# Kernel optimization log

Measured on AMD Instinct MI355X. Metric: run time of the kernel, lower is better.

## Reference

```python
import math
import jax, jax.numpy as jnp
import numpy as np

B, Q, K, D, H, C = 4, 1024, 1024, 256, 8, 32  # batch, q_len, kv_len, model dim, heads, per-head dim


def setup_inputs() -> dict:
    key = jax.random.key(0)
    ks = jax.random.split(key, 9)
    s = 1.0 / math.sqrt(D)
    return {
        "q_x": jax.random.normal(ks[0], (B, Q, D), jnp.float32),
        "kv_x": jax.random.normal(ks[1], (B, K, D), jnp.float32),
        "bias_mask": jax.random.normal(ks[2], (B, 1, 1, K), jnp.float32),
        "bias_pair": jax.random.normal(ks[3], (B, H, Q, K), jnp.float32),
        "wq": jax.random.normal(ks[4], (D, H * C), jnp.float32) * s,
        "wk": jax.random.normal(ks[5], (D, H * C), jnp.float32) * s,
        "wv": jax.random.normal(ks[6], (D, H * C), jnp.float32) * s,
        "wg": jnp.zeros((D, H * C), jnp.float32),  # gating init: weights 0
        "bg": jnp.ones((H * C,), jnp.float32),     # gating init: bias 1
        "wo": jax.random.normal(ks[7], (H * C, D), jnp.float32) * s,
        "bo": jnp.zeros((D,), jnp.float32),
    }


def reference(q_x, kv_x, bias_mask, bias_pair, wq, wk, wv, wg, bg, wo, bo):
    # project and split heads: [B, L, H, C]
    q = (q_x @ wq).reshape(B, Q, H, C) / math.sqrt(C)
    k = (kv_x @ wk).reshape(B, K, H, C)
    v = (kv_x @ wv).reshape(B, K, H, C)
    # scores [B, H, Q, K] with multiple additive biases
    scores = jnp.einsum("bqhc,bkhc->bhqk", q, k) + bias_mask + bias_pair
    a = jax.nn.softmax(scores, axis=-1)
    o = jnp.einsum("bhqk,bkhc->bqhc", a, v).reshape(B, Q, H * C)
    # sigmoid gate from query activations
    g = jax.nn.sigmoid(q_x @ wg + bg)
    o = o * g
    return o @ wo + bo
```

## Files before the change

### kernel.cpp

```cpp
#include <hip/hip_runtime.h>
#include <hip/hip_bf16.h>


typedef short bf16x8 __attribute__((ext_vector_type(8)));
typedef float f32x4 __attribute__((ext_vector_type(4)));

__device__ __forceinline__ unsigned short f2bf(float f) {
  __hip_bfloat16 hb = __float2bfloat16(f);
  return *reinterpret_cast<const unsigned short*>(&hb);
}

__global__ __launch_bounds__(256) void transpose_conv(
    const float* __restrict__ wq, const float* __restrict__ wk,
    const float* __restrict__ wv, const float* __restrict__ wg,
    const float* __restrict__ wo, unsigned short* __restrict__ wt) {
  __shared__ float t[64][65];
  const int widx = blockIdx.x >> 4;
  const int tile = blockIdx.x & 15;
  const float* src = widx == 0 ? wq : widx == 1 ? wk
                     : widx == 2 ? wv : widx == 3 ? wg : wo;
  unsigned short* dst = wt + widx * 65536;
  const int r0 = (tile >> 2) * 64, c0 = (tile & 3) * 64;
  const int tr = threadIdx.x >> 4;
  const int tc4 = (threadIdx.x & 15) * 4;
#pragma unroll
  for (int i = 0; i < 4; ++i) {
    const float4 u = *reinterpret_cast<const float4*>(
        src + (size_t)(r0 + tr + i * 16) * 256 + c0 + tc4);
    t[tr + i * 16][tc4 + 0] = u.x;
    t[tr + i * 16][tc4 + 1] = u.y;
    t[tr + i * 16][tc4 + 2] = u.z;
    t[tr + i * 16][tc4 + 3] = u.w;
  }
  __syncthreads();
#pragma unroll
  for (int i = 0; i < 4; ++i) {
    const int rr = tr + i * 16;
    ushort4 o;
    o.x = f2bf(t[tc4 + 0][rr]);
    o.y = f2bf(t[tc4 + 1][rr]);
    o.z = f2bf(t[tc4 + 2][rr]);
    o.w = f2bf(t[tc4 + 3][rr]);
    *reinterpret_cast<ushort4*>(dst + (size_t)(c0 + rr) * 256 + r0 + tc4) = o;
  }
}

__global__ __launch_bounds__(256) void proj_mfma(
    const float* __restrict__ q_x, const float* __restrict__ kv_x,
    const unsigned short* __restrict__ wt, const float* __restrict__ bg,
    unsigned short* __restrict__ qhb, unsigned short* __restrict__ khb,
    unsigned short* __restrict__ vhb, float* __restrict__ gws) {
  const int side = blockIdx.y;
  const int m0 = blockIdx.x * 16;
  const int lane = threadIdx.x & 63;
  const int n0 = (threadIdx.x >> 6) * 64;
  const int mrow = lane & 15;
  const int quad = lane >> 4;
  const float* X = side ? kv_x : q_x;
  const unsigned short* W0 = wt + (side ? 1 : 0) * 65536;
  const unsigned short* W1 = wt + (side ? 2 : 3) * 65536;
  f32x4 acc0[4], acc1[4];
  const f32x4 z = {0.f, 0.f, 0.f, 0.f};
#pragma unroll
  for (int nt = 0; nt < 4; ++nt) { acc0[nt] = z; acc1[nt] = z; }

  for (int k0 = 0; k0 < 256; k0 += 32) {
    const size_t abase = (size_t)(m0 + mrow) * 256 + k0 + quad * 8;
    const float4 a0 = *reinterpret_cast<const float4*>(X + abase);
    const float4 a1 = *reinterpret_cast<const float4*>(X + abase + 4);
    bf16x8 a;
    a[0] = (short)f2bf(a0.x); a[1] = (short)f2bf(a0.y);
    a[2] = (short)f2bf(a0.z); a[3] = (short)f2bf(a0.w);
    a[4] = (short)f2bf(a1.x); a[5] = (short)f2bf(a1.y);
    a[6] = (short)f2bf(a1.z); a[7] = (short)f2bf(a1.w);
#pragma unroll
    for (int nt = 0; nt < 4; ++nt) {
      const size_t wrow = (size_t)(n0 + nt * 16 + mrow) * 256 + k0 + quad * 8;
      const bf16x8 b0 = *reinterpret_cast<const bf16x8*>(W0 + wrow);
      const bf16x8 b1 = *reinterpret_cast<const bf16x8*>(W1 + wrow);
      acc0[nt] = __builtin_amdgcn_mfma_f32_16x16x32_bf16(a, b0, acc0[nt], 0, 0, 0);
      acc1[nt] = __builtin_amdgcn_mfma_f32_16x16x32_bf16(a, b1, acc1[nt], 0, 0, 0);
    }
  }

  const int b = m0 >> 10;
#pragma unroll
  for (int nt = 0; nt < 4; ++nt) {
    const int n = n0 + nt * 16 + mrow;
    const int h = n >> 5, c = n & 31;
    const float bgv = (side == 0) ? bg[n] : 0.f;
#pragma unroll
    for (int r = 0; r < 4; ++r) {
      const int row = m0 + quad * 4 + r;
      const int qp = row & 1023;
      const size_t o = ((size_t)(b * 8 + h) * 1024 + qp) * 32 + c;
      if (side == 0) {
        qhb[o] = f2bf(acc0[nt][r] * 0.17677669529663689f);
        const float zz = acc1[nt][r] + bgv;
        gws[(size_t)row * 256 + n] = 1.0f / (1.0f + __expf(-zz));
      } else {
        khb[o] = f2bf(acc0[nt][r]);
        vhb[o] = f2bf(acc1[nt][r]);
      }
    }
  }
}

__global__ __launch_bounds__(256) void attn_mfma(
    const unsigned short* __restrict__ qhb,
    const unsigned short* __restrict__ khb,
    const unsigned short* __restrict__ vhb,
    const float* __restrict__ bias_mask,
    const float* __restrict__ bias_pair,
    const float* __restrict__ gws, unsigned short* __restrict__ og) {
  __shared__ unsigned short ks[64 * 40];
  __shared__ unsigned short vsT[32 * 72];
  __shared__ unsigned short ps[64 * 72];
  const int x = blockIdx.x;
  const int b = x >> 7, h = (x >> 4) & 7, q0 = (x & 15) * 64;
  const int tid = threadIdx.x;
  const int wv = tid >> 6, lane = tid & 63, quad = lane >> 4, lr = lane & 15;
  const int bh = b * 8 + h;

  const bf16x8 aq = *reinterpret_cast<const bf16x8*>(
      qhb + ((size_t)bh * 1024 + q0 + wv * 16 + lr) * 32 + quad * 8);

  float m[4], l[4];
  f32x4 oa[2];
  const f32x4 zero4 = {0.f, 0.f, 0.f, 0.f};
  oa[0] = zero4; oa[1] = zero4;
#pragma unroll
  for (int r = 0; r < 4; ++r) { m[r] = -3e30f; l[r] = 0.f; }

  const float* bp = bias_pair + ((size_t)bh * 1024 + q0 + wv * 16) * 1024;
  const float* bm = bias_mask + (size_t)b * 1024;

  for (int kt = 0; kt < 16; ++kt) {
    const int kk0 = kt * 64;
    __syncthreads();
    {
      const unsigned short* ksrc = khb + (size_t)bh * 32768 + kk0 * 32;
      const int row = tid >> 2, c8 = (tid & 3) * 8;
      *reinterpret_cast<bf16x8*>(ks + row * 40 + c8) =
          *reinterpret_cast<const bf16x8*>(ksrc + row * 32 + c8);
      const unsigned short* vsrc = vhb + (size_t)bh * 32768 + kk0 * 32;
      const bf16x8 vv = *reinterpret_cast<const bf16x8*>(vsrc + row * 32 + c8);
#pragma unroll
      for (int i = 0; i < 8; ++i) vsT[(c8 + i) * 72 + row] = (unsigned short)vv[i];
    }
    __syncthreads();

    f32x4 s[4];
    float mk[4];
#pragma unroll
    for (int nt = 0; nt < 4; ++nt) mk[nt] = bm[kk0 + 16 * nt + lr];
#pragma unroll
    for (int nt = 0; nt < 4; ++nt) {
#pragma unroll
      for (int r = 0; r < 4; ++r)
        s[nt][r] = bp[(size_t)(quad * 4 + r) * 1024 + kk0 + 16 * nt + lr] + mk[nt];
      const bf16x8 bk = *reinterpret_cast<const bf16x8*>(
          ks + (16 * nt + lr) * 40 + quad * 8);
      s[nt] = __builtin_amdgcn_mfma_f32_16x16x32_bf16(aq, bk, s[nt], 0, 0, 0);
    }

#pragma unroll
    for (int r = 0; r < 4; ++r) {
      float mx = fmaxf(fmaxf(s[0][r], s[1][r]), fmaxf(s[2][r], s[3][r]));
      mx = fmaxf(mx, __shfl_xor(mx, 1));
      mx = fmaxf(mx, __shfl_xor(mx, 2));
      mx = fmaxf(mx, __shfl_xor(mx, 4));
      mx = fmaxf(mx, __shfl_xor(mx, 8));
      const float mn = fmaxf(m[r], mx);
      const float alpha = __expf(m[r] - mn);
      float rs = 0.f;
#pragma unroll
      for (int nt = 0; nt < 4; ++nt) {
        s[nt][r] = __expf(s[nt][r] - mn);
        rs += s[nt][r];
      }
      rs += __shfl_xor(rs, 1);
      rs += __shfl_xor(rs, 2);
      rs += __shfl_xor(rs, 4);
      rs += __shfl_xor(rs, 8);
      l[r] = l[r] * alpha + rs;
      m[r] = mn;
      oa[0][r] *= alpha;
      oa[1][r] *= alpha;
      const int ri = wv * 16 + quad * 4 + r;
#pragma unroll
      for (int nt = 0; nt < 4; ++nt)
        ps[ri * 72 + 16 * nt + lr] = f2bf(s[nt][r]);
    }
    asm volatile("s_waitcnt lgkmcnt(0)" ::: "memory");

#pragma unroll
    for (int k0i = 0; k0i < 2; ++k0i) {
      const bf16x8 ap = *reinterpret_cast<const bf16x8*>(
          ps + (wv * 16 + lr) * 72 + k0i * 32 + quad * 8);
#pragma unroll
      for (int nt2 = 0; nt2 < 2; ++nt2) {
        const bf16x8 bv = *reinterpret_cast<const bf16x8*>(
            vsT + (nt2 * 16 + lr) * 72 + k0i * 32 + quad * 8);
        oa[nt2] = __builtin_amdgcn_mfma_f32_16x16x32_bf16(ap, bv, oa[nt2], 0, 0, 0);
      }
    }
  }

#pragma unroll
  for (int r = 0; r < 4; ++r) {
    const int qr = q0 + wv * 16 + quad * 4 + r;
    const float inv = 1.0f / l[r];
    const size_t base = ((size_t)b * 1024 + qr) * 256 + h * 32;
#pragma unroll
    for (int nt2 = 0; nt2 < 2; ++nt2) {
      const int c = nt2 * 16 + lr;
      og[base + c] = f2bf(oa[nt2][r] * inv * gws[base + c]);
    }
  }
}

__global__ __launch_bounds__(256) void outproj_mfma(
    const unsigned short* __restrict__ og,
    const unsigned short* __restrict__ wt,
    const float* __restrict__ bo, float* __restrict__ out) {
  const int m0 = blockIdx.x * 16;
  const int lane = threadIdx.x & 63;
  const int n0 = (threadIdx.x >> 6) * 64;
  const int mrow = lane & 15;
  const int quad = lane >> 4;
  const unsigned short* W = wt + 4 * 65536;
  f32x4 acc[4];
  const f32x4 z = {0.f, 0.f, 0.f, 0.f};
#pragma unroll
  for (int nt = 0; nt < 4; ++nt) acc[nt] = z;

  for (int k0 = 0; k0 < 256; k0 += 32) {
    const bf16x8 a = *reinterpret_cast<const bf16x8*>(
        og + (size_t)(m0 + mrow) * 256 + k0 + quad * 8);
#pragma unroll
    for (int nt = 0; nt < 4; ++nt) {
      const bf16x8 b = *reinterpret_cast<const bf16x8*>(
          W + (size_t)(n0 + nt * 16 + mrow) * 256 + k0 + quad * 8);
      acc[nt] = __builtin_amdgcn_mfma_f32_16x16x32_bf16(a, b, acc[nt], 0, 0, 0);
    }
  }

#pragma unroll
  for (int nt = 0; nt < 4; ++nt) {
    const int n = n0 + nt * 16 + mrow;
    const float bov = bo[n];
#pragma unroll
    for (int r = 0; r < 4; ++r) {
      const int row = m0 + quad * 4 + r;
      out[(size_t)row * 256 + n] = acc[nt][r] + bov;
    }
  }
}

extern "C" void kernel_launch(void* const* d_in, const int* in_sizes, int n_in,
                              void* d_out, int out_size, void* d_ws,
                              size_t ws_size, hipStream_t stream) {
  (void)in_sizes; (void)n_in; (void)out_size; (void)ws_size;
  const float* q_x = (const float*)d_in[0];
  const float* kv_x = (const float*)d_in[1];
  const float* bias_mask = (const float*)d_in[2];
  const float* bias_pair = (const float*)d_in[3];
  const float* wq = (const float*)d_in[4];
  const float* wk = (const float*)d_in[5];
  const float* wv = (const float*)d_in[6];
  const float* wg = (const float*)d_in[7];
  const float* bg = (const float*)d_in[8];
  const float* wo = (const float*)d_in[9];
  const float* bo = (const float*)d_in[10];

  char* wsb = (char*)d_ws;
  unsigned short* wt  = (unsigned short*)(wsb);
  unsigned short* qhb = (unsigned short*)(wsb + 655360);
  unsigned short* khb = (unsigned short*)(wsb + 2752512);
  unsigned short* vhb = (unsigned short*)(wsb + 4849664);
  unsigned short* og  = (unsigned short*)(wsb + 6946816);
  float* gws          = (float*)(wsb + 9043968);

  transpose_conv<<<80, 256, 0, stream>>>(wq, wk, wv, wg, wo, wt);
  proj_mfma<<<dim3(256, 2), 256, 0, stream>>>(q_x, kv_x, wt, bg, qhb, khb,
                                              vhb, gws);
  attn_mfma<<<512, 256, 0, stream>>>(qhb, khb, vhb, bias_mask, bias_pair, gws,
                                     og);
  outproj_mfma<<<256, 256, 0, stream>>>(og, wt, bo, (float*)d_out);
}
```

Before: 252.9 us.

## Store V transposed and load K/V fragments directly from global in attention

The projection kernel now writes V in a [bh, c, k] transposed layout. The attention kernel drops the shared-memory staging of K and V, and with it both __syncthreads per tile. Each wave reads K and V MFMA operands straight from global memory (L2-cached) and keeps only a private per-wave P buffer in LDS. This removes block-level barriers and the LDS transpose. The cost is redundant global loads across the four waves and strided scattered stores of V in the projection.

```diff
diff --git a/kernel.cpp b/kernel.cpp
--- a/kernel.cpp
+++ b/kernel.cpp
@@ -49,7 +49,7 @@
     const float* __restrict__ q_x, const float* __restrict__ kv_x,
     const unsigned short* __restrict__ wt, const float* __restrict__ bg,
     unsigned short* __restrict__ qhb, unsigned short* __restrict__ khb,
-    unsigned short* __restrict__ vhb, float* __restrict__ gws) {
+    unsigned short* __restrict__ vhT, float* __restrict__ gws) {
   const int side = blockIdx.y;
   const int m0 = blockIdx.x * 16;
   const int lane = threadIdx.x & 63;
@@ -88,19 +88,20 @@
   for (int nt = 0; nt < 4; ++nt) {
     const int n = n0 + nt * 16 + mrow;
     const int h = n >> 5, c = n & 31;
+    const int bh = b * 8 + h;
     const float bgv = (side == 0) ? bg[n] : 0.f;
 #pragma unroll
     for (int r = 0; r < 4; ++r) {
       const int row = m0 + quad * 4 + r;
       const int qp = row & 1023;
-      const size_t o = ((size_t)(b * 8 + h) * 1024 + qp) * 32 + c;
       if (side == 0) {
-        qhb[o] = f2bf(acc0[nt][r] * 0.17677669529663689f);
+        qhb[((size_t)bh * 1024 + qp) * 32 + c] =
+            f2bf(acc0[nt][r] * 0.17677669529663689f);
         const float zz = acc1[nt][r] + bgv;
         gws[(size_t)row * 256 + n] = 1.0f / (1.0f + __expf(-zz));
       } else {
-        khb[o] = f2bf(acc0[nt][r]);
-        vhb[o] = f2bf(acc1[nt][r]);
+        khb[((size_t)bh * 1024 + qp) * 32 + c] = f2bf(acc0[nt][r]);
+        vhT[((size_t)bh * 32 + c) * 1024 + qp] = f2bf(acc1[nt][r]);
       }
     }
   }
@@ -109,21 +110,21 @@
 __global__ __launch_bounds__(256) void attn_mfma(
     const unsigned short* __restrict__ qhb,
     const unsigned short* __restrict__ khb,
-    const unsigned short* __restrict__ vhb,
+    const unsigned short* __restrict__ vhT,
     const float* __restrict__ bias_mask,
     const float* __restrict__ bias_pair,
     const float* __restrict__ gws, unsigned short* __restrict__ og) {
-  __shared__ unsigned short ks[64 * 40];
-  __shared__ unsigned short vsT[32 * 72];
-  __shared__ unsigned short ps[64 * 72];
+  __shared__ unsigned short ps[4 * 16 * 72];
   const int x = blockIdx.x;
-  const int b = x >> 7, h = (x >> 4) & 7, q0 = (x & 15) * 64;
+  const int b = x >> 7, h = (x >> 4) & 7;
   const int tid = threadIdx.x;
   const int wv = tid >> 6, lane = tid & 63, quad = lane >> 4, lr = lane & 15;
   const int bh = b * 8 + h;
+  const int q0 = (x & 15) * 64 + wv * 16;
+  unsigned short* psw = ps + wv * 16 * 72;
 
   const bf16x8 aq = *reinterpret_cast<const bf16x8*>(
-      qhb + ((size_t)bh * 1024 + q0 + wv * 16 + lr) * 32 + quad * 8);
+      qhb + ((size_t)bh * 1024 + q0 + lr) * 32 + quad * 8);
 
   float m[4], l[4];
   f32x4 oa[2];
@@ -132,35 +133,27 @@
 #pragma unroll
   for (int r = 0; r < 4; ++r) { m[r] = -3e30f; l[r] = 0.f; }
 
-  const float* bp = bias_pair + ((size_t)bh * 1024 + q0 + wv * 16) * 1024;
+  const float* bp = bias_pair + ((size_t)bh * 1024 + q0) * 1024;
   const float* bm = bias_mask + (size_t)b * 1024;
+  const unsigned short* kbase = khb + (size_t)bh * 32768;
+  const unsigned short* vbase = vhT + (size_t)bh * 32768;
 
   for (int kt = 0; kt < 16; ++kt) {
     const int kk0 = kt * 64;
-    __syncthreads();
-    {
-      const unsigned short* ksrc = khb + (size_t)bh * 32768 + kk0 * 32;
-      const int row = tid >> 2, c8 = (tid & 3) * 8;
-      *reinterpret_cast<bf16x8*>(ks + row * 40 + c8) =
-          *reinterpret_cast<const bf16x8*>(ksrc + row * 32 + c8);
-      const unsigned short* vsrc = vhb + (size_t)bh * 32768 + kk0 * 32;
-      const bf16x8 vv = *reinterpret_cast<const bf16x8*>(vsrc + row * 32 + c8);
-#pragma unroll
-      for (int i = 0; i < 8; ++i) vsT[(c8 + i) * 72 + row] = (unsigned short)vv[i];
-    }
-    __syncthreads();
 
     f32x4 s[4];
-    float mk[4];
-#pragma unroll
-    for (int nt = 0; nt < 4; ++nt) mk[nt] = bm[kk0 + 16 * nt + lr];
-#pragma unroll
-    for (int nt = 0; nt < 4; ++nt) {
+#pragma unroll
+    for (int nt = 0; nt < 4; ++nt) {
+      const int kcol = kk0 + 16 * nt + lr;
+      const float mk = bm[kcol];
 #pragma unroll
       for (int r = 0; r < 4; ++r)
-        s[nt][r] = bp[(size_t)(quad * 4 + r) * 1024 + kk0 + 16 * nt + lr] + mk[nt];
+        s[nt][r] = bp[(size_t)(quad * 4 + r) * 1024 + kcol] + mk;
+    }
+#pragma unroll
+    for (int nt = 0; nt < 4; ++nt) {
       const bf16x8 bk = *reinterpret_cast<const bf16x8*>(
-          ks + (16 * nt + lr) * 40 + quad * 8);
+          kbase + (size_t)(kk0 + 16 * nt + lr) * 32 + quad * 8);
       s[nt] = __builtin_amdgcn_mfma_f32_16x16x32_bf16(aq, bk, s[nt], 0, 0, 0);
     }
 
@@ -187,21 +180,21 @@
       m[r] = mn;
       oa[0][r] *= alpha;
       oa[1][r] *= alpha;
-      const int ri = wv * 16 + quad * 4 + r;
+      const int ri = quad * 4 + r;
 #pragma unroll
       for (int nt = 0; nt < 4; ++nt)
-        ps[ri * 72 + 16 * nt + lr] = f2bf(s[nt][r]);
+        psw[ri * 72 + 16 * nt + lr] = f2bf(s[nt][r]);
     }
     asm volatile("s_waitcnt lgkmcnt(0)" ::: "memory");
 
 #pragma unroll
     for (int k0i = 0; k0i < 2; ++k0i) {
       const bf16x8 ap = *reinterpret_cast<const bf16x8*>(
-          ps + (wv * 16 + lr) * 72 + k0i * 32 + quad * 8);
+          psw + lr * 72 + k0i * 32 + quad * 8);
 #pragma unroll
       for (int nt2 = 0; nt2 < 2; ++nt2) {
         const bf16x8 bv = *reinterpret_cast<const bf16x8*>(
-            vsT + (nt2 * 16 + lr) * 72 + k0i * 32 + quad * 8);
+            vbase + (size_t)(nt2 * 16 + lr) * 1024 + kk0 + k0i * 32 + quad * 8);
         oa[nt2] = __builtin_amdgcn_mfma_f32_16x16x32_bf16(ap, bv, oa[nt2], 0, 0, 0);
       }
     }
@@ -209,7 +202,7 @@
 
 #pragma unroll
   for (int r = 0; r < 4; ++r) {
-    const int qr = q0 + wv * 16 + quad * 4 + r;
+    const int qr = q0 + quad * 4 + r;
     const float inv = 1.0f / l[r];
     const size_t base = ((size_t)b * 1024 + qr) * 256 + h * 32;
 #pragma unroll
@@ -278,14 +271,14 @@
   unsigned short* wt  = (unsigned short*)(wsb);
   unsigned short* qhb = (unsigned short*)(wsb + 655360);
   unsigned short* khb = (unsigned short*)(wsb + 2752512);
-  unsigned short* vhb = (unsigned short*)(wsb + 4849664);
+  unsigned short* vhT = (unsigned short*)(wsb + 4849664);
   unsigned short* og  = (unsigned short*)(wsb + 6946816);
   float* gws          = (float*)(wsb + 9043968);
 
   transpose_conv<<<80, 256, 0, stream>>>(wq, wk, wv, wg, wo, wt);
   proj_mfma<<<dim3(256, 2), 256, 0, stream>>>(q_x, kv_x, wt, bg, qhb, khb,
-                                              vhb, gws);
-  attn_mfma<<<512, 256, 0, stream>>>(qhb, khb, vhb, bias_mask, bias_pair, gws,
+                                              vhT, gws);
+  attn_mfma<<<512, 256, 0, stream>>>(qhb, khb, vhT, bias_mask, bias_pair, gws,
                                      og);
   outproj_mfma<<<256, 256, 0, stream>>>(og, wt, bo, (float*)d_out);
 }
```

Result: slower. 260.3 us (+2.9%).
